# Kernel tuning notes

Hardware: AMD Instinct MI355X
Metric: run time of the kernel (lower is better)

The kernel has to match this reference:

```python
import jax, jax.numpy as jnp
import numpy as np

B, T, D, H = 1, 2048, 1024, 16
HS = D // H  # 64
FF = 4 * D   # 4096
EPS = 1e-6


def rmsnorm(x, w):
    xf = x.astype(jnp.float32)
    n = xf * jax.lax.rsqrt(jnp.mean(xf * xf, axis=-1, keepdims=True) + EPS)
    return n.astype(x.dtype) * w


def setup_inputs() -> dict:
    key = jax.random.key(0)
    ks = jax.random.split(key, 9)
    s = 0.02
    return {
        "x": jax.random.normal(ks[0], (B, T, D), jnp.float32),
        "Wq": jax.random.normal(ks[1], (H, D, HS), jnp.float32) * s,
        "Wk": jax.random.normal(ks[2], (H, D, HS), jnp.float32) * s,
        "Wv": jax.random.normal(ks[3], (H, D, HS), jnp.float32) * s,
        "Wproj": jax.random.normal(ks[4], (H * HS, D), jnp.float32) * s,
        "bproj": jnp.zeros((D,), jnp.float32),
        "W1": jax.random.normal(ks[5], (D, FF), jnp.float32) * s,
        "W2": jax.random.normal(ks[6], (FF, D), jnp.float32) * s,
        "g1": jnp.ones((D,), jnp.float32),
        "g2": jnp.ones((D,), jnp.float32),
    }


def reference(x, Wq, Wk, Wv, Wproj, bproj, W1, W2, g1, g2):
    # --- self attention on RMSNorm(x) ---
    xn = rmsnorm(x, g1)                                   # [B,T,D]
    q = jnp.einsum('btd,hds->bhts', xn, Wq)               # [B,H,T,hs]
    k = jnp.einsum('btd,hds->bhts', xn, Wk)
    v = jnp.einsum('btd,hds->bhts', xn, Wv)
    scale = HS ** -0.5
    wei = jnp.einsum('bhts,bhus->bhtu', q, k) * scale     # [B,H,T,T]
    causal = jnp.tril(jnp.ones((T, T), bool))
    wei = jnp.where(causal, wei, -jnp.inf)
    wei = jax.nn.softmax(wei, axis=-1)
    attn = jnp.einsum('bhtu,bhus->bhts', wei, v)          # [B,H,T,hs]
    attn = attn.transpose(0, 2, 1, 3).reshape(B, T, H * HS)
    sa = attn @ Wproj + bproj                             # [B,T,D]
    x = x + sa
    # --- SiLU FFN on RMSNorm(x) ---
    xn2 = rmsnorm(x, g2)
    h = jax.nn.silu(xn2 @ W1)                             # [B,T,4D]
    x = x + h @ W2
    return x
```

## Files before the change

### kernel.cpp

```cpp
#include <hip/hip_runtime.h>

typedef unsigned short u16;
typedef unsigned int u32;
typedef __attribute__((ext_vector_type(4))) float f32x4;
typedef __attribute__((ext_vector_type(8))) __bf16 bf16x8;

#define T_SEQ 2048
#define DMODEL 1024
#define NHEAD 16
#define HEADS 64
#define FFDIM 4096
#define MNQ 2097152l

__device__ __forceinline__ u16 f2bf(float f) {
  u32 u = __builtin_bit_cast(u32, f);
  u = u + 0x7FFFu + ((u >> 16) & 1u);
  return (u16)(u >> 16);
}
__device__ __forceinline__ float bf2f(u16 h) {
  u32 u = ((u32)h) << 16;
  return __builtin_bit_cast(float, u);
}
__device__ __forceinline__ void gload_lds16(const u16* g, u16* l) {
  __builtin_amdgcn_global_load_lds(
      (const __attribute__((address_space(1))) u32*)g,
      (__attribute__((address_space(3))) u32*)l, 16, 0, 0);
}

__global__ __launch_bounds__(256) void prep_k(
    const float* __restrict__ Wq, const float* __restrict__ Wk,
    const float* __restrict__ Wv, const float* __restrict__ Wproj,
    const float* __restrict__ W1, const float* __restrict__ W2,
    const float* __restrict__ x, const float* __restrict__ g1,
    u16* __restrict__ QKVwT, u16* __restrict__ WprojT,
    u16* __restrict__ W1T, u16* __restrict__ W2T, u16* __restrict__ xn1) {
  __shared__ u16 tile[64 * 66];
  __shared__ float wsum[4];
  int bid = blockIdx.x;
  int tid = threadIdx.x;
  if (bid >= 3072) {
    int row = bid - 3072;
    const float4* xr = (const float4*)(x + (long)row * DMODEL);
    float4 v = xr[tid];
    float ss = v.x * v.x + v.y * v.y + v.z * v.z + v.w * v.w;
#pragma unroll
    for (int off = 32; off >= 1; off >>= 1) ss += __shfl_xor(ss, off, 64);
    if ((tid & 63) == 0) wsum[tid >> 6] = ss;
    __syncthreads();
    float tot = wsum[0] + wsum[1] + wsum[2] + wsum[3];
    float rms = rsqrtf(tot * (1.0f / DMODEL) + 1e-6f);
    float4 gv = ((const float4*)g1)[tid];
    ushort4 o4 = make_ushort4(f2bf(v.x * rms * gv.x), f2bf(v.y * rms * gv.y),
                              f2bf(v.z * rms * gv.z), f2bf(v.w * rms * gv.w));
    ((ushort4*)(xn1 + (long)row * DMODEL))[tid] = o4;
    return;
  }
  const float* in;
  u16* out;
  long ldin, ldout;
  int r0, c0;
  if (bid < 768) {
    int z = bid >> 4, xi = bid & 15;
    int wsel = z >> 4, h = z & 15;
    in = (wsel == 0 ? Wq : (wsel == 1 ? Wk : Wv)) + (long)h * 65536;
    out = QKVwT + (long)wsel * 1048576 + (long)h * 65536;
    ldin = 64; ldout = 1024;
    r0 = xi * 64; c0 = 0;
  } else if (bid < 1024) {
    int b = bid - 768;
    in = Wproj; out = WprojT; ldin = 1024; ldout = 1024;
    r0 = (b >> 4) * 64; c0 = (b & 15) * 64;
  } else if (bid < 2048) {
    int b = bid - 1024;
    in = W1; out = W1T; ldin = 4096; ldout = 1024;
    r0 = (b & 15) * 64; c0 = (b >> 4) * 64;
  } else {
    int b = bid - 2048;
    in = W2; out = W2T; ldin = 1024; ldout = 4096;
    r0 = (b >> 4) * 64; c0 = (b & 15) * 64;
  }
#pragma unroll
  for (int p = 0; p < 16; ++p) {
    int idx = p * 256 + tid;
    int r = idx >> 6, c = idx & 63;
    tile[c * 66 + r] = f2bf(in[(long)(r0 + r) * ldin + c0 + c]);
  }
  __syncthreads();
#pragma unroll
  for (int p = 0; p < 16; ++p) {
    int idx = p * 256 + tid;
    int c = idx >> 6, r = idx & 63;
    out[(long)(c0 + c) * ldout + r0 + r] = tile[c * 66 + r];
  }
}

__global__ __launch_bounds__(256) void proj_rms_k(
    const u16* __restrict__ part, const float* __restrict__ bias,
    const float* __restrict__ resid, const float* __restrict__ g,
    float* __restrict__ x1, u16* __restrict__ xn2) {
  int row = blockIdx.x;
  int tid = threadIdx.x;
  long i = (long)row * DMODEL + tid * 4;
  float4 r = *(const float4*)(resid + i);
  float4 bi = *(const float4*)(bias + tid * 4);
  float4 v;
  v.x = r.x + bi.x; v.y = r.y + bi.y; v.z = r.z + bi.z; v.w = r.w + bi.w;
#pragma unroll
  for (int z = 0; z < 4; ++z) {
    ushort4 a = *(const ushort4*)(part + z * MNQ + i);
    v.x += bf2f(a.x); v.y += bf2f(a.y); v.z += bf2f(a.z); v.w += bf2f(a.w);
  }
  *(float4*)(x1 + i) = v;
  float ss = v.x * v.x + v.y * v.y + v.z * v.z + v.w * v.w;
#pragma unroll
  for (int off = 32; off >= 1; off >>= 1) ss += __shfl_xor(ss, off, 64);
  __shared__ float wsum[4];
  if ((tid & 63) == 0) wsum[tid >> 6] = ss;
  __syncthreads();
  float tot = wsum[0] + wsum[1] + wsum[2] + wsum[3];
  float rms = rsqrtf(tot * (1.0f / DMODEL) + 1e-6f);
  float4 gv = ((const float4*)g)[tid];
  ushort4 o4 = make_ushort4(f2bf(v.x * rms * gv.x), f2bf(v.y * rms * gv.y),
                            f2bf(v.z * rms * gv.z), f2bf(v.w * rms * gv.w));
  ((ushort4*)(xn2 + (long)row * DMODEL))[tid] = o4;
}

template <int EPI>
__global__ __launch_bounds__(256, 4) void gemm_bt_k(
    const u16* __restrict__ A, const u16* __restrict__ Bt, int N, int K, int kc,
    u16* __restrict__ out16, u16* __restrict__ vt, u16* __restrict__ part) {
  __shared__ __align__(16) u16 As[2][128 * 32];
  __shared__ __align__(16) u16 Bs[2][64 * 32];
  int tid = threadIdx.x;
  int w = tid >> 6, lane = tid & 63;
  int quad = lane >> 4, l15 = lane & 15;
  int m0 = blockIdx.x * 128, n0 = blockIdx.y * 64;
  int kz = blockIdx.z;
  int wr = w >> 1, wc = w & 1;

  f32x4 acc[4][2] = {};

  int lr = lane >> 2, lc = (lane & 3) * 8;
  const u16* AgL = A + (long)(m0 + w * 32 + lr) * K + lc;
  const u16* BgL = Bt + (long)(n0 + w * 16 + lr) * K + lc;
  u16* AsW[2] = {As[0] + w * 1024, As[1] + w * 1024};
  u16* BsW[2] = {Bs[0] + w * 512, Bs[1] + w * 512};

  int kbeg = kz * kc, kend = kbeg + kc;

  gload_lds16(AgL + kbeg, AsW[0]);
  gload_lds16(AgL + 16 * K + kbeg, AsW[0] + 512);
  gload_lds16(BgL + kbeg, BsW[0]);
  __syncthreads();

  int buf = 0;
  for (int kb = kbeg; kb < kend; kb += 32) {
    bool more = (kb + 32 < kend);
    if (more) {
      int nb = buf ^ 1;
      gload_lds16(AgL + kb + 32, AsW[nb]);
      gload_lds16(AgL + 16 * K + kb + 32, AsW[nb] + 512);
      gload_lds16(BgL + kb + 32, BsW[nb]);
    }
    bf16x8 af[4], bfr[2];
#pragma unroll
    for (int mt = 0; mt < 4; ++mt)
      af[mt] = *(const bf16x8*)(As[buf] + (wr * 64 + mt * 16 + l15) * 32 + quad * 8);
#pragma unroll
    for (int nt = 0; nt < 2; ++nt)
      bfr[nt] = *(const bf16x8*)(Bs[buf] + (wc * 32 + nt * 16 + l15) * 32 + quad * 8);
#pragma unroll
    for (int mt = 0; mt < 4; ++mt)
#pragma unroll
      for (int nt = 0; nt < 2; ++nt)
        acc[mt][nt] = __builtin_amdgcn_mfma_f32_16x16x32_bf16(
            af[mt], bfr[nt], acc[mt][nt], 0, 0, 0);
    if (more) __syncthreads();
    buf ^= 1;
  }

  bool vblock = (EPI == 0) && (vt != nullptr) && (n0 >= 2048);
  u16* pb = nullptr;
  if (EPI == 4) pb = part + (long)kz * MNQ;
#pragma unroll
  for (int mt = 0; mt < 4; ++mt)
#pragma unroll
    for (int nt = 0; nt < 2; ++nt) {
      int col = n0 + wc * 32 + nt * 16 + l15;
      if (EPI == 0 && vblock) {
        int s = col - 2048;
        int row0 = m0 + wr * 64 + mt * 16 + quad * 4;
        ushort4 pk = make_ushort4(f2bf(acc[mt][nt][0]), f2bf(acc[mt][nt][1]),
                                  f2bf(acc[mt][nt][2]), f2bf(acc[mt][nt][3]));
        *(ushort4*)(vt + (long)s * 2048 + row0) = pk;
        continue;
      }
#pragma unroll
      for (int r = 0; r < 4; ++r) {
        int row = m0 + wr * 64 + mt * 16 + quad * 4 + r;
        long idx = (long)row * N + col;
        float v = acc[mt][nt][r];
        if (EPI == 0) {
          out16[idx] = f2bf(v);
        } else if (EPI == 2) {
          out16[idx] = f2bf(v / (1.0f + __expf(-v)));
        } else if (EPI == 4) {
          pb[idx] = f2bf(v);
        }
      }
    }
}

__global__ __launch_bounds__(256) void reduce_ffn2_k(
    const u16* __restrict__ part, const float* __restrict__ resid,
    float* __restrict__ out) {
  long i = ((long)blockIdx.x * 256 + threadIdx.x) * 4;
  float4 r = *(const float4*)(resid + i);
  float4 o = r;
#pragma unroll
  for (int z = 0; z < 4; ++z) {
    ushort4 a = *(const ushort4*)(part + z * MNQ + i);
    o.x += bf2f(a.x); o.y += bf2f(a.y); o.z += bf2f(a.z); o.w += bf2f(a.w);
  }
  *(float4*)(out + i) = o;
}

#define LSTR 72
__global__ __launch_bounds__(256) void attn_part_k(const u16* __restrict__ QKV,
                                                   const u16* __restrict__ Vt,
                                                   u16* __restrict__ Opart,
                                                   float* __restrict__ lpart) {
  __shared__ __align__(16) u16 Qs[64 * LSTR];
  __shared__ __align__(16) u16 Ks[64 * LSTR];
  __shared__ __align__(16) u16 Vs[64 * LSTR];
  __shared__ float lbuf[64];

  int tid = threadIdx.x;
  int w = tid >> 6, lane = tid & 63;
  int quad = lane >> 4, l15 = lane & 15;
  int h = blockIdx.y;

  int p = blockIdx.x;
  int bx = 0, acc0 = 0;
  while (true) {
    int n = (bx >> 3) + 1;
    if (p < acc0 + n) break;
    acc0 += n;
    ++bx;
  }
  int c = p - acc0;
  int t0 = bx * 64;
  int jstart = c * 8;
  int jend = min(jstart + 8, bx + 1);

#pragma unroll
  for (int pp = 0; pp < 2; ++pp) {
    int idx = pp * 256 + tid;
    int row = idx >> 3, cc = idx & 7;
    *(uint4*)(Qs + row * LSTR + cc * 8) =
        *(const uint4*)(QKV + (long)(t0 + row) * 3072 + h * 64 + cc * 8);
  }
  __syncthreads();
  bf16x8 aq[2];
#pragma unroll
  for (int ks = 0; ks < 2; ++ks)
    aq[ks] = *(const bf16x8*)(Qs + (w * 16 + l15) * LSTR + ks * 32 + quad * 8);

  f32x4 oacc[4] = {};
  float lsum = 0.f;
  int qg = t0 + w * 16 + l15;

  u16* PsW = Qs + w * (16 * LSTR);

  for (int j = jstart; j < jend; ++j) {
    __syncthreads();
#pragma unroll
    for (int pp = 0; pp < 2; ++pp) {
      int idx = pp * 256 + tid;
      int row = idx >> 3, cc = idx & 7;
      *(uint4*)(Ks + row * LSTR + cc * 8) =
          *(const uint4*)(QKV + (long)(j * 64 + row) * 3072 + 1024 + h * 64 + cc * 8);
      *(uint4*)(Vs + row * LSTR + cc * 8) =
          *(const uint4*)(Vt + (long)h * (64 * 2048) + (long)row * 2048 + j * 64 + cc * 8);
    }
    __syncthreads();

    f32x4 sacc[4] = {};
#pragma unroll
    for (int ks = 0; ks < 2; ++ks)
#pragma unroll
      for (int ut = 0; ut < 4; ++ut) {
        bf16x8 kf = *(const bf16x8*)(Ks + (ut * 16 + l15) * LSTR + ks * 32 + quad * 8);
        sacc[ut] = __builtin_amdgcn_mfma_f32_16x16x32_bf16(kf, aq[ks], sacc[ut], 0, 0, 0);
      }

    bool boundary = (j == bx);
#pragma unroll
    for (int ut = 0; ut < 4; ++ut) {
      float pv[4];
#pragma unroll
      for (int r = 0; r < 4; ++r) {
        float v = exp2f(sacc[ut][r] * 0.18033688f);
        if (boundary) {
          int u = j * 64 + ut * 16 + quad * 4 + r;
          if (u > qg) v = 0.f;
        }
        pv[r] = v;
        lsum += v;
      }
      ushort4 pk = make_ushort4(f2bf(pv[0]), f2bf(pv[1]), f2bf(pv[2]), f2bf(pv[3]));
      *(ushort4*)(PsW + l15 * LSTR + ut * 16 + quad * 4) = pk;
    }
    asm volatile("s_waitcnt lgkmcnt(0)" ::: "memory");
#pragma unroll
    for (int ks = 0; ks < 2; ++ks) {
      bf16x8 pf = *(const bf16x8*)(PsW + l15 * LSTR + ks * 32 + quad * 8);
#pragma unroll
      for (int ct = 0; ct < 4; ++ct) {
        bf16x8 vf = *(const bf16x8*)(Vs + (ct * 16 + l15) * LSTR + ks * 32 + quad * 8);
        oacc[ct] = __builtin_amdgcn_mfma_f32_16x16x32_bf16(pf, vf, oacc[ct], 0, 0, 0);
      }
    }
  }

  lsum += __shfl_xor(lsum, 16, 64);
  lsum += __shfl_xor(lsum, 32, 64);
  if (quad == 0) lbuf[w * 16 + l15] = 1.0f / lsum;
  asm volatile("s_waitcnt lgkmcnt(0)" ::: "memory");

  long slot = (long)p * 16 + h;
  float inv[4];
#pragma unroll
  for (int r = 0; r < 4; ++r) inv[r] = lbuf[w * 16 + quad * 4 + r];
  u16* Ob = Opart + slot * 4096;
#pragma unroll
  for (int ct = 0; ct < 4; ++ct)
#pragma unroll
    for (int r = 0; r < 4; ++r)
      Ob[(w * 16 + quad * 4 + r) * 64 + ct * 16 + l15] = f2bf(oacc[ct][r] * inv[r]);
  if (quad == 0) lpart[slot * 64 + w * 16 + l15] = lsum;
}

__global__ __launch_bounds__(256) void attn_combine_k(
    const u16* __restrict__ Opart, const float* __restrict__ lpart,
    u16* __restrict__ out) {
  int bx = blockIdx.x, h = blockIdx.y;
  int g = bx >> 3;
  int p0 = 4 * g * (g + 1) + (bx - 8 * g) * (g + 1);
  int nc = g + 1;
  int tid = threadIdx.x;
  int row = tid >> 2, c4 = (tid & 3) * 16;

  float lv[4];
  float wsum = 0.f;
  for (int cidx = 0; cidx < nc; ++cidx) {
    long slot = (long)(p0 + cidx) * 16 + h;
    lv[cidx] = lpart[slot * 64 + row];
    wsum += lv[cidx];
  }
  float rinv = 1.0f / wsum;

  float o[16];
#pragma unroll
  for (int i = 0; i < 16; ++i) o[i] = 0.f;
  for (int cidx = 0; cidx < nc; ++cidx) {
    float wc = lv[cidx] * rinv;
    const u16* Ob = Opart + ((long)(p0 + cidx) * 16 + h) * 4096 + row * 64 + c4;
    bf16x8 a = *(const bf16x8*)Ob;
    bf16x8 b = *(const bf16x8*)(Ob + 8);
#pragma unroll
    for (int i = 0; i < 8; ++i) {
      o[i] += wc * (float)a[i];
      o[8 + i] += wc * (float)b[i];
    }
  }
  u16 ob[16];
#pragma unroll
  for (int i = 0; i < 16; ++i) ob[i] = f2bf(o[i]);
  u16* op = out + (long)(bx * 64 + row) * 1024 + h * 64 + c4;
  *(uint4*)op = *(uint4*)ob;
  *(uint4*)(op + 8) = *(uint4*)(ob + 8);
}

extern "C" void kernel_launch(void* const* d_in, const int* in_sizes, int n_in,
                              void* d_out, int out_size, void* d_ws, size_t ws_size,
                              hipStream_t stream) {
  const float* x     = (const float*)d_in[0];
  const float* Wq    = (const float*)d_in[1];
  const float* Wk    = (const float*)d_in[2];
  const float* Wv    = (const float*)d_in[3];
  const float* Wproj = (const float*)d_in[4];
  const float* bproj = (const float*)d_in[5];
  const float* W1    = (const float*)d_in[6];
  const float* W2    = (const float*)d_in[7];
  const float* g1    = (const float*)d_in[8];
  const float* g2    = (const float*)d_in[9];

  char* ws = (char*)d_ws;
  u16* QKVwT  = (u16*)(ws);
  u16* WprojT = (u16*)(ws + (6ul << 20));
  u16* W1T    = (u16*)(ws + (8ul << 20));
  u16* W2T    = (u16*)(ws + (16ul << 20));
  u16* xn1    = (u16*)(ws + (24ul << 20));
  u16* QKVb   = (u16*)(ws + (28ul << 20));
  u16* VtB    = (u16*)(ws + (40ul << 20));
  u16* attn   = (u16*)(ws + (44ul << 20));
  float* x1   = (float*)(ws + (48ul << 20));
  u16* xn2    = (u16*)(ws + (56ul << 20));
  u16* hbuf   = (u16*)(ws + (60ul << 20));
  u16* Opart    = (u16*)(ws + (48ul << 20));
  float* lpart  = (float*)(ws + (58ul << 20));
  u16* projp    = (u16*)(ws + (28ul << 20));
  u16* ffn2p    = (u16*)(ws + (28ul << 20));
  if (ws_size < (76ul << 20)) return;

  dim3 blk(256);

  prep_k<<<dim3(5120), blk, 0, stream>>>(
      Wq, Wk, Wv, Wproj, W1, W2, x, g1, QKVwT, WprojT, W1T, W2T, xn1);
  gemm_bt_k<0><<<dim3(16, 48, 1), blk, 0, stream>>>(
      xn1, QKVwT, 3072, 1024, 1024, QKVb, VtB, nullptr);
  attn_part_k<<<dim3(80, 16), blk, 0, stream>>>(QKVb, VtB, Opart, lpart);
  attn_combine_k<<<dim3(32, 16), blk, 0, stream>>>(Opart, lpart, attn);
  gemm_bt_k<4><<<dim3(16, 16, 4), blk, 0, stream>>>(
      attn, WprojT, 1024, 1024, 256, nullptr, nullptr, projp);
  proj_rms_k<<<dim3(2048), blk, 0, stream>>>(projp, bproj, x, g2, x1, xn2);
  gemm_bt_k<2><<<dim3(16, 64, 1), blk, 0, stream>>>(
      xn2, W1T, 4096, 1024, 1024, hbuf, nullptr, nullptr);
  gemm_bt_k<4><<<dim3(16, 16, 4), blk, 0, stream>>>(
      hbuf, W2T, 1024, 4096, 1024, nullptr, nullptr, ffn2p);
  reduce_ffn2_k<<<dim3(2048), blk, 0, stream>>>(ffn2p, x1, (float*)d_out);
}
```

Before: 255.9 us.

## Triple-buffer GEMM LDS tiles with vmcnt-based waits and one barrier per iteration

Moves the bf16 GEMM main loop from double to triple buffering in LDS. Loads are issued two k-steps ahead. A partial s_waitcnt vmcnt(3) plus a single barrier per iteration replaces the full __syncthreads at both ends. The goal is to hide global-to-LDS load latency better and remove one barrier per step, at the cost of 50% more LDS per block, which could lower occupancy under launch_bounds(256,4).

After: 257.5 us. Within noise of the previous version (+0.6%).

```diff
diff --git a/kernel.cpp b/kernel.cpp
--- a/kernel.cpp
+++ b/kernel.cpp
@@ -129,8 +129,8 @@
 __global__ __launch_bounds__(256, 4) void gemm_bt_k(
     const u16* __restrict__ A, const u16* __restrict__ Bt, int N, int K, int kc,
     u16* __restrict__ out16, u16* __restrict__ vt, u16* __restrict__ part) {
-  __shared__ __align__(16) u16 As[2][128 * 32];
-  __shared__ __align__(16) u16 Bs[2][64 * 32];
+  __shared__ __align__(16) u16 As[3][128 * 32];
+  __shared__ __align__(16) u16 Bs[3][64 * 32];
   int tid = threadIdx.x;
   int w = tid >> 6, lane = tid & 63;
   int quad = lane >> 4, l15 = lane & 15;
@@ -141,42 +141,49 @@
   f32x4 acc[4][2] = {};
 
   int lr = lane >> 2, lc = (lane & 3) * 8;
-  const u16* AgL = A + (long)(m0 + w * 32 + lr) * K + lc;
-  const u16* BgL = Bt + (long)(n0 + w * 16 + lr) * K + lc;
-  u16* AsW[2] = {As[0] + w * 1024, As[1] + w * 1024};
-  u16* BsW[2] = {Bs[0] + w * 512, Bs[1] + w * 512};
-
-  int kbeg = kz * kc, kend = kbeg + kc;
-
-  gload_lds16(AgL + kbeg, AsW[0]);
-  gload_lds16(AgL + 16 * K + kbeg, AsW[0] + 512);
-  gload_lds16(BgL + kbeg, BsW[0]);
-  __syncthreads();
-
-  int buf = 0;
-  for (int kb = kbeg; kb < kend; kb += 32) {
-    bool more = (kb + 32 < kend);
-    if (more) {
-      int nb = buf ^ 1;
-      gload_lds16(AgL + kb + 32, AsW[nb]);
-      gload_lds16(AgL + 16 * K + kb + 32, AsW[nb] + 512);
-      gload_lds16(BgL + kb + 32, BsW[nb]);
-    }
+  const u16* Ak = A + (long)(m0 + w * 32 + lr) * K + lc + (long)kz * kc;
+  const u16* A2k = Ak + (long)16 * K;
+  const u16* Bk = Bt + (long)(n0 + w * 16 + lr) * K + lc + (long)kz * kc;
+  u16* Aw[3] = {As[0] + w * 1024, As[1] + w * 1024, As[2] + w * 1024};
+  u16* Bw[3] = {Bs[0] + w * 512, Bs[1] + w * 512, Bs[2] + w * 512};
+
+  int niter = kc >> 5;
+
+  gload_lds16(Ak, Aw[0]);
+  gload_lds16(A2k, Aw[0] + 512);
+  gload_lds16(Bk, Bw[0]);
+  gload_lds16(Ak + 32, Aw[1]);
+  gload_lds16(A2k + 32, Aw[1] + 512);
+  gload_lds16(Bk + 32, Bw[1]);
+
+  int cb = 0;
+  for (int k = 0; k < niter; ++k) {
+    if (k + 2 < niter) {
+      asm volatile("s_waitcnt vmcnt(3)\n\ts_barrier" ::: "memory");
+      int pb = (cb == 0) ? 2 : cb - 1;
+      int off = (k + 2) * 32;
+      gload_lds16(Ak + off, Aw[pb]);
+      gload_lds16(A2k + off, Aw[pb] + 512);
+      gload_lds16(Bk + off, Bw[pb]);
+    } else {
+      asm volatile("s_waitcnt vmcnt(0)\n\ts_barrier" ::: "memory");
+    }
+    const u16* Ab = As[cb];
+    const u16* Bb = Bs[cb];
     bf16x8 af[4], bfr[2];
 #pragma unroll
     for (int mt = 0; mt < 4; ++mt)
-      af[mt] = *(const bf16x8*)(As[buf] + (wr * 64 + mt * 16 + l15) * 32 + quad * 8);
+      af[mt] = *(const bf16x8*)(Ab + (wr * 64 + mt * 16 + l15) * 32 + quad * 8);
 #pragma unroll
     for (int nt = 0; nt < 2; ++nt)
-      bfr[nt] = *(const bf16x8*)(Bs[buf] + (wc * 32 + nt * 16 + l15) * 32 + quad * 8);
+      bfr[nt] = *(const bf16x8*)(Bb + (wc * 32 + nt * 16 + l15) * 32 + quad * 8);
 #pragma unroll
     for (int mt = 0; mt < 4; ++mt)
 #pragma unroll
       for (int nt = 0; nt < 2; ++nt)
         acc[mt][nt] = __builtin_amdgcn_mfma_f32_16x16x32_bf16(
             af[mt], bfr[nt], acc[mt][nt], 0, 0, 0);
-    if (more) __syncthreads();
-    buf ^= 1;
+    cb = (cb == 2) ? 0 : cb + 1;
   }
 
   bool vblock = (EPI == 0) && (vt != nullptr) && (n0 >= 2048);
```
